# Optimization experiments

Measured on AMD Instinct MI355X. Metric: run time of the kernel, lower is better.

## Reference

```python
import jax, jax.numpy as jnp
import numpy as np

N_NODES = 10000
IN_CH = 512
HID = 128
HEADS = 4
OUT_CH = 256
N_EDGES = 160000
NEG_SLOPE = 0.2  # PyG GATConv default


def gat_conv(x, src, dst, W, a_src, a_dst, b):
    """PyG-style GATConv. x:[N,F_in], W:[F_in,H*C], a_src/a_dst:[H,C], b:[H*C].
    src/dst already include self-loops. Returns [N, H*C] (concat heads)."""
    N = x.shape[0]
    H, C = a_src.shape
    h = (x @ W).reshape(N, H, C)                     # [N,H,C]
    e_src = jnp.einsum('nhc,hc->nh', h, a_src)        # [N,H]
    e_dst = jnp.einsum('nhc,hc->nh', h, a_dst)
    alpha = jax.nn.leaky_relu(e_src[src] + e_dst[dst], NEG_SLOPE)  # [E,H]
    # softmax over incoming edges of each destination node
    m = jax.ops.segment_max(alpha, dst, num_segments=N)            # [N,H]
    ex = jnp.exp(alpha - m[dst])
    denom = jax.ops.segment_sum(ex, dst, num_segments=N)           # [N,H]
    coeff = ex / (denom[dst] + 1e-16)                              # [E,H]
    out = jax.ops.segment_sum(coeff[:, :, None] * h[src], dst, num_segments=N)  # [N,H,C]
    return out.reshape(N, H * C) + b


def _edges_with_self_loops(edge_index, n):
    loops = jnp.arange(n, dtype=edge_index.dtype)
    src = jnp.concatenate([edge_index[0], loops])
    dst = jnp.concatenate([edge_index[1], loops])
    return src, dst


def setup_inputs() -> dict:
    key = jax.random.key(0)
    ks = jax.random.split(key, 20)
    s = 0.05
    inp = {
        'x': jax.random.normal(ks[0], (N_NODES, IN_CH), jnp.float32),
        'W1': jax.random.normal(ks[1], (IN_CH, HEADS * HID), jnp.float32) * s,
        'a1s': jax.random.normal(ks[2], (HEADS, HID), jnp.float32) * s,
        'a1d': jax.random.normal(ks[3], (HEADS, HID), jnp.float32) * s,
        'b1': jnp.zeros((HEADS * HID,), jnp.float32),
        'W2': jax.random.normal(ks[4], (HEADS * HID, HEADS * HID), jnp.float32) * s,
        'a2s': jax.random.normal(ks[5], (HEADS, HID), jnp.float32) * s,
        'a2d': jax.random.normal(ks[6], (HEADS, HID), jnp.float32) * s,
        'b2': jnp.zeros((HEADS * HID,), jnp.float32),
        'W3': jax.random.normal(ks[7], (HEADS * HID, HID), jnp.float32) * s,
        'a3s': jax.random.normal(ks[8], (1, HID), jnp.float32) * s,
        'a3d': jax.random.normal(ks[9], (1, HID), jnp.float32) * s,
        'b3': jnp.zeros((HID,), jnp.float32),
        'Wl': jax.random.normal(ks[10], (HID, OUT_CH), jnp.float32) * s,
        'bl': jnp.zeros((OUT_CH,), jnp.float32),
        'Wr': jax.random.normal(ks[11], (IN_CH, OUT_CH), jnp.float32) * s,
        'br': jnp.zeros((OUT_CH,), jnp.float32),
        'edge_index': jax.random.randint(ks[12], (2, N_EDGES), 0, N_NODES, jnp.int64 if jax.config.jax_enable_x64 else jnp.int32),
    }
    return inp


def reference(x, W1, a1s, a1d, b1, W2, a2s, a2d, b2, W3, a3s, a3d, b3, Wl, bl, Wr, br, edge_index):
    src, dst = _edges_with_self_loops(edge_index, x.shape[0])
    residual = x @ Wr + br
    h = jax.nn.elu(gat_conv(x, src, dst, W1, a1s, a1d, b1))
    h = jax.nn.elu(gat_conv(h, src, dst, W2, a2s, a2d, b2))
    h = jax.nn.elu(gat_conv(h, src, dst, W3, a3s, a3d, b3))
    return h @ Wl + bl + residual
```

## Files before the change

kernel.cpp:

```cpp
#include <hip/hip_runtime.h>
#include <hip/hip_bf16.h>
#include <cstdint>
#include <cstddef>

#define N_NODES 10000
#define M_PAD   10112
#define HEADS   4

typedef __bf16 bfrag8 __attribute__((ext_vector_type(8)));
typedef __bf16 bfrag2 __attribute__((ext_vector_type(2)));
typedef float  floatx4 __attribute__((ext_vector_type(4)));
typedef float  floatx2 __attribute__((ext_vector_type(2)));

#define S0V (M_PAD * 512 / 8)
#define S1 (512 * 512)
#define S2 (512 * 512)
#define S3 (512 * 128)
#define S4 (128 * 256)
#define S5 (512 * 256)

__global__ __launch_bounds__(256) void prep(const float* __restrict__ x,
                                            const float* __restrict__ W1,
                                            const float* __restrict__ W2,
                                            const float* __restrict__ W3,
                                            const float* __restrict__ Wl,
                                            const float* __restrict__ Wr,
                                            const int* __restrict__ edst, int E,
                                            __bf16* __restrict__ xb,
                                            __bf16* __restrict__ W1T,
                                            __bf16* __restrict__ W2T,
                                            __bf16* __restrict__ W3T,
                                            __bf16* __restrict__ WlT,
                                            __bf16* __restrict__ WrT,
                                            int* __restrict__ deg) {
    int i = blockIdx.x * 256 + threadIdx.x;
    if (i < S0V) {
        int base = i * 8;
        int row = base >> 9;
        bfrag8 r = {};
        if (row < N_NODES) {
            float4 f0 = ((const float4*)x)[i * 2];
            float4 f1 = ((const float4*)x)[i * 2 + 1];
            r[0] = (__bf16)f0.x; r[1] = (__bf16)f0.y; r[2] = (__bf16)f0.z; r[3] = (__bf16)f0.w;
            r[4] = (__bf16)f1.x; r[5] = (__bf16)f1.y; r[6] = (__bf16)f1.z; r[7] = (__bf16)f1.w;
        }
        *(bfrag8*)(xb + base) = r;
    } else if ((i -= S0V) < S1) {
        int k = i >> 9, n = i & 511;
        W1T[n * 512 + k] = (__bf16)W1[i];
    } else if ((i -= S1) < S2) {
        int k = i >> 9, n = i & 511;
        W2T[n * 512 + k] = (__bf16)W2[i];
    } else if ((i -= S2) < S3) {
        int k = i >> 7, n = i & 127;
        W3T[n * 512 + k] = (__bf16)W3[i];
    } else if ((i -= S3) < S4) {
        int k = i >> 8, n = i & 255;
        WlT[n * 128 + k] = (__bf16)Wl[i];
    } else if ((i -= S4) < S5) {
        int k = i >> 8, n = i & 255;
        WrT[n * 512 + k] = (__bf16)Wr[i];
    } else if ((i -= S5) < E) {
        atomicAdd(&deg[edst[i]], 1);
    }
}


__global__ __launch_bounds__(256) void scan_kernel(const int* __restrict__ deg,
                                                   int* __restrict__ rowptr,
                                                   int* __restrict__ cursor, int n) {
    __shared__ int wtot[4], woff[4];
    int t = threadIdx.x, lane = t & 63, wv = t >> 6;
    int chunk = (n + 255) / 256;
    int beg = t * chunk, end = beg + chunk; if (end > n) end = n; if (beg > n) beg = n;
    int s = 0;
    for (int i = beg; i < end; ++i) s += deg[i] + 1;
    int v = s;
#pragma unroll
    for (int off = 1; off < 64; off <<= 1) {
        int o = __shfl_up(v, off);
        if (lane >= off) v += o;
    }
    if (lane == 63) wtot[wv] = v;
    __syncthreads();
    if (t == 0) {
        int r = 0;
#pragma unroll
        for (int i = 0; i < 4; ++i) { woff[i] = r; r += wtot[i]; }
        rowptr[n] = r;
    }
    __syncthreads();
    int off = woff[wv] + v - s;
    for (int i = beg; i < end; ++i) {
        rowptr[i] = off; cursor[i] = off;
        off += deg[i] + 1;
    }
}

__global__ __launch_bounds__(256) void scatter_kernel(const int* __restrict__ src,
                                                      const int* __restrict__ dst, int E, int n,
                                                      int* __restrict__ cursor,
                                                      int* __restrict__ csr) {
    int i = blockIdx.x * 256 + threadIdx.x;
    if (i < E) {
        int pos = atomicAdd(&cursor[dst[i]], 1);
        csr[pos] = src[i];
    } else if (i < E + n) {
        int v = i - E;
        int pos = atomicAdd(&cursor[v], 1);
        csr[pos] = v;
    }
}


template <int NT>
__device__ __forceinline__ void gemm_loop(const __bf16* __restrict__ A,
                                          const __bf16* __restrict__ BT, int K,
                                          int m0, int n0, int wave, int lane,
                                          __bf16* As, __bf16* Bs,
                                          floatx4 (&acc)[2][NT]) {
    int r = wave * 8 + (lane >> 3);
    int kof = (lane & 7) * 8;
    const __bf16* gA = A + (size_t)(m0 + r) * K + kof;
    const __bf16* gB = BT + (size_t)(n0 + r) * K + kof;
    __bf16* lA = As + r * 64 + kof;
    __bf16* lB = Bs + r * 64 + kof;
    const __bf16* fA = As + (wave * 32 + (lane & 15)) * 64 + (lane >> 4) * 8;
    const __bf16* fB = Bs + (lane & 15) * 64 + (lane >> 4) * 8;

    for (int k0 = 0; k0 < K; k0 += 64) {
#pragma unroll
        for (int u = 0; u < 4; ++u)
            __builtin_amdgcn_global_load_lds(
                (const __attribute__((address_space(1))) void*)(gA + (size_t)u * 32 * K),
                (__attribute__((address_space(3))) void*)(lA + u * 32 * 64), 16, 0, 0);
#pragma unroll
        for (int u = 0; u < NT / 2; ++u)
            __builtin_amdgcn_global_load_lds(
                (const __attribute__((address_space(1))) void*)(gB + (size_t)u * 32 * K),
                (__attribute__((address_space(3))) void*)(lB + u * 32 * 64), 16, 0, 0);
        gA += 64; gB += 64;
        __syncthreads();

#pragma unroll
        for (int ks = 0; ks < 2; ++ks) {
            bfrag8 a0 = *(const bfrag8*)(fA + ks * 32);
            bfrag8 a1 = *(const bfrag8*)(fA + 16 * 64 + ks * 32);
#pragma unroll
            for (int nt = 0; nt < NT; ++nt) {
                bfrag8 b = *(const bfrag8*)(fB + nt * 16 * 64 + ks * 32);
                acc[0][nt] = __builtin_amdgcn_mfma_f32_16x16x32_bf16(a0, b, acc[0][nt], 0, 0, 0);
                acc[1][nt] = __builtin_amdgcn_mfma_f32_16x16x32_bf16(a1, b, acc[1][nt], 0, 0, 0);
            }
        }
        __syncthreads();
    }
}

__global__ __launch_bounds__(256) void gemm_h(const __bf16* __restrict__ A,
                                              const __bf16* __restrict__ BT,
                                              __bf16* __restrict__ Cb,
                                              unsigned char* __restrict__ C8,
                                              int N, int K) {
    __shared__ __align__(16) __bf16 As[128 * 64];
    __shared__ __align__(16) __bf16 Bs[64 * 64];
    int tid = threadIdx.x, wave = tid >> 6, lane = tid & 63;
    int n0 = blockIdx.x * 64, m0 = blockIdx.y * 128;
    floatx4 acc[2][4] = {};
    gemm_loop<4>(A, BT, K, m0, n0, wave, lane, As, Bs, acc);

    int crow = m0 + wave * 32 + (lane >> 4) * 4;
    int ccol = n0 + (lane & 15);
#pragma unroll
    for (int mt = 0; mt < 2; ++mt)
#pragma unroll
        for (int nt = 0; nt < 4; ++nt)
#pragma unroll
            for (int r = 0; r < 4; ++r) {
                float v = acc[mt][nt][r];
                size_t o = (size_t)(crow + mt * 16 + r) * N + ccol + nt * 16;
                Cb[o] = (__bf16)v;
                int p = __builtin_amdgcn_cvt_pk_fp8_f32(v, v, 0, false);
                C8[o] = (unsigned char)(p & 0xff);
            }
}

__global__ __launch_bounds__(256) void gemm_final(const __bf16* __restrict__ A1,
                                                  const __bf16* __restrict__ B1T, int K1,
                                                  const __bf16* __restrict__ A2,
                                                  const __bf16* __restrict__ B2T, int K2,
                                                  float* __restrict__ C,
                                                  const float* __restrict__ bias1,
                                                  const float* __restrict__ bias2,
                                                  int M, int N) {
    __shared__ __align__(16) __bf16 As[128 * 64];
    __shared__ __align__(16) __bf16 Bs[64 * 64];
    int tid = threadIdx.x, wave = tid >> 6, lane = tid & 63;
    int n0 = blockIdx.x * 64, m0 = blockIdx.y * 128;
    floatx4 acc[2][4] = {};
    gemm_loop<4>(A1, B1T, K1, m0, n0, wave, lane, As, Bs, acc);
    gemm_loop<4>(A2, B2T, K2, m0, n0, wave, lane, As, Bs, acc);

    int crow = m0 + wave * 32 + (lane >> 4) * 4;
    int ccol = n0 + (lane & 15);
#pragma unroll
    for (int mt = 0; mt < 2; ++mt)
#pragma unroll
        for (int nt = 0; nt < 4; ++nt)
#pragma unroll
            for (int r = 0; r < 4; ++r) {
                int row = crow + mt * 16 + r;
                int col = ccol + nt * 16;
                if (row < M)
                    C[(size_t)row * N + col] = acc[mt][nt][r] + bias1[col] + bias2[col];
            }
}


template <int H>
__global__ __launch_bounds__(256) void attn_e(const __bf16* __restrict__ Hb,
                                              const float* __restrict__ as_,
                                              const float* __restrict__ ad_,
                                              float* __restrict__ es,
                                              float* __restrict__ ed) {
    constexpr int F = H * 128;
    constexpr int GROUP = (H == 4) ? 16 : 64;
    int wave = threadIdx.x >> 6, lane = threadIdx.x & 63;
    int node = blockIdx.x * 4 + wave;
    if (node >= N_NODES) return;
    float ps = 0.f, pd = 0.f;
    if (H == 4) {
        bfrag8 v = *(const bfrag8*)(Hb + (size_t)node * F + lane * 8);
#pragma unroll
        for (int k = 0; k < 8; ++k) {
            float f = (float)v[k];
            ps += f * as_[lane * 8 + k];
            pd += f * ad_[lane * 8 + k];
        }
    } else {
        bfrag2 v = *(const bfrag2*)(Hb + (size_t)node * F + lane * 2);
#pragma unroll
        for (int k = 0; k < 2; ++k) {
            float f = (float)v[k];
            ps += f * as_[lane * 2 + k];
            pd += f * ad_[lane * 2 + k];
        }
    }
#pragma unroll
    for (int off = GROUP / 2; off; off >>= 1) {
        ps += __shfl_down(ps, off);
        pd += __shfl_down(pd, off);
    }
    if ((lane & (GROUP - 1)) == 0) {
        es[node * H + lane / GROUP] = ps;
        ed[node * H + lane / GROUP] = pd;
    }
}


template <int H>
__global__ __launch_bounds__(256) void gather_agg(const unsigned char* __restrict__ H8,
                                                  const float* __restrict__ es,
                                                  const float* __restrict__ ed,
                                                  const int* __restrict__ rowptr,
                                                  const int* __restrict__ csr,
                                                  const float* __restrict__ bias,
                                                  __bf16* __restrict__ outb) {
    constexpr int F = H * 128;
    constexpr int CH = F / 64;
    int wave = threadIdx.x >> 6, lane = threadIdx.x & 63;
    int node = blockIdx.x * 4 + wave;
    if (node >= M_PAD) return;
    int hsel = (H == 4) ? (lane >> 4) : 0;
    __bf16* op = outb + (size_t)node * F + lane * CH;
    if (node >= N_NODES) {
        if (H == 4) { bfrag8 z = {}; *(bfrag8*)op = z; }
        else        { bfrag2 z = {}; *(bfrag2*)op = z; }
        return;
    }
    const unsigned char* hp = H8 + lane * CH;
    float edv = ed[node * H + hsel];
    int beg = rowptr[node], end = rowptr[node + 1];
    float acc[CH] = {};
    float wsum = 0.f;
    int j = beg;
    for (; j + 7 < end; j += 8) {
        int s[8];
        float e[8];
#pragma unroll
        for (int u = 0; u < 8; ++u) s[u] = csr[j + u];
#pragma unroll
        for (int u = 0; u < 8; ++u) e[u] = es[s[u] * H + hsel];
        if (H == 4) {
            uint2 p[8];
#pragma unroll
            for (int u = 0; u < 8; ++u) p[u] = *(const uint2*)(hp + (size_t)s[u] * F);
#pragma unroll
            for (int u = 0; u < 8; ++u) {
                float t = e[u] + edv;
                t = t > 0.f ? t : 0.2f * t;
                float wgt = __expf(t);
                wsum += wgt;
                floatx2 f0 = __builtin_amdgcn_cvt_pk_f32_fp8(p[u].x, false);
                floatx2 f1 = __builtin_amdgcn_cvt_pk_f32_fp8(p[u].x, true);
                floatx2 f2 = __builtin_amdgcn_cvt_pk_f32_fp8(p[u].y, false);
                floatx2 f3 = __builtin_amdgcn_cvt_pk_f32_fp8(p[u].y, true);
                acc[0] += wgt * f0[0]; acc[1] += wgt * f0[1];
                acc[2] += wgt * f1[0]; acc[3] += wgt * f1[1];
                acc[4] += wgt * f2[0]; acc[5] += wgt * f2[1];
                acc[6] += wgt * f3[0]; acc[7] += wgt * f3[1];
            }
        } else {
            unsigned short p[8];
#pragma unroll
            for (int u = 0; u < 8; ++u) p[u] = *(const unsigned short*)(hp + (size_t)s[u] * F);
#pragma unroll
            for (int u = 0; u < 8; ++u) {
                float t = e[u] + edv;
                t = t > 0.f ? t : 0.2f * t;
                float wgt = __expf(t);
                wsum += wgt;
                floatx2 f0 = __builtin_amdgcn_cvt_pk_f32_fp8((int)p[u], false);
                acc[0] += wgt * f0[0]; acc[1] += wgt * f0[1];
            }
        }
    }
    for (; j < end; ++j) {
        int s0 = csr[j];
        float t = es[s0 * H + hsel] + edv;
        t = t > 0.f ? t : 0.2f * t;
        float wgt = __expf(t);
        wsum += wgt;
        if (H == 4) {
            uint2 p = *(const uint2*)(hp + (size_t)s0 * F);
            floatx2 f0 = __builtin_amdgcn_cvt_pk_f32_fp8(p.x, false);
            floatx2 f1 = __builtin_amdgcn_cvt_pk_f32_fp8(p.x, true);
            floatx2 f2 = __builtin_amdgcn_cvt_pk_f32_fp8(p.y, false);
            floatx2 f3 = __builtin_amdgcn_cvt_pk_f32_fp8(p.y, true);
            acc[0] += wgt * f0[0]; acc[1] += wgt * f0[1];
            acc[2] += wgt * f1[0]; acc[3] += wgt * f1[1];
            acc[4] += wgt * f2[0]; acc[5] += wgt * f2[1];
            acc[6] += wgt * f3[0]; acc[7] += wgt * f3[1];
        } else {
            unsigned short p = *(const unsigned short*)(hp + (size_t)s0 * F);
            floatx2 f0 = __builtin_amdgcn_cvt_pk_f32_fp8((int)p, false);
            acc[0] += wgt * f0[0]; acc[1] += wgt * f0[1];
        }
    }
    float inv = 1.f / (wsum + 1e-16f);
    if (H == 4) {
        bfrag8 r;
#pragma unroll
        for (int k = 0; k < 8; ++k) {
            float o = acc[k] * inv + bias[lane * 8 + k];
            o = o > 0.f ? o : __expf(o) - 1.f;
            r[k] = (__bf16)o;
        }
        *(bfrag8*)op = r;
    } else {
        bfrag2 r;
#pragma unroll
        for (int k = 0; k < 2; ++k) {
            float o = acc[k] * inv + bias[lane * 2 + k];
            o = o > 0.f ? o : __expf(o) - 1.f;
            r[k] = (__bf16)o;
        }
        *(bfrag2*)op = r;
    }
}


extern "C" void kernel_launch(void* const* d_in, const int* in_sizes, int n_in,
                              void* d_out, int out_size, void* d_ws, size_t ws_size,
                              hipStream_t stream) {
    const float* x   = (const float*)d_in[0];
    const float* W1  = (const float*)d_in[1];
    const float* a1s = (const float*)d_in[2];
    const float* a1d = (const float*)d_in[3];
    const float* b1  = (const float*)d_in[4];
    const float* W2  = (const float*)d_in[5];
    const float* a2s = (const float*)d_in[6];
    const float* a2d = (const float*)d_in[7];
    const float* b2  = (const float*)d_in[8];
    const float* W3  = (const float*)d_in[9];
    const float* a3s = (const float*)d_in[10];
    const float* a3d = (const float*)d_in[11];
    const float* b3  = (const float*)d_in[12];
    const float* Wl  = (const float*)d_in[13];
    const float* bl  = (const float*)d_in[14];
    const float* Wr  = (const float*)d_in[15];
    const float* br  = (const float*)d_in[16];
    const int*   ei  = (const int*)d_in[17];
    const int E = in_sizes[17] / 2;
    const int* esrc = ei;
    const int* edst = ei + E;
    const int slots = E + N_NODES;
    float* out = (float*)d_out;

    char* w = (char*)d_ws;
    auto alloc = [&](size_t b) { char* p = w; w += (b + 255) & ~(size_t)255; return p; };
    __bf16* xb  = (__bf16*)alloc((size_t)M_PAD * 512 * 2);
    __bf16* hb  = (__bf16*)alloc((size_t)M_PAD * 512 * 2);
    __bf16* hb3 = (__bf16*)alloc((size_t)M_PAD * 128 * 2);
    __bf16* Hib = (__bf16*)alloc((size_t)M_PAD * 512 * 2);
    unsigned char* Hi8 = (unsigned char*)alloc((size_t)M_PAD * 512);
    __bf16* W1T = (__bf16*)alloc(512 * 512 * 2);
    __bf16* W2T = (__bf16*)alloc(512 * 512 * 2);
    __bf16* W3T = (__bf16*)alloc(128 * 512 * 2);
    __bf16* WlT = (__bf16*)alloc(256 * 128 * 2);
    __bf16* WrT = (__bf16*)alloc(256 * 512 * 2);
    float* es     = (float*)alloc(N_NODES * HEADS * 4);
    float* ed     = (float*)alloc(N_NODES * HEADS * 4);
    int*   deg    = (int*)alloc(N_NODES * 4);
    int*   rowptr = (int*)alloc((N_NODES + 1) * 4);
    int*   cursor = (int*)alloc(N_NODES * 4);
    int*   csr    = (int*)alloc((size_t)slots * 4);

    (void)hipMemsetAsync(deg, 0, N_NODES * sizeof(int), stream);

    const int sp_total = S0V + S1 + S2 + S3 + S4 + S5 + E;
    prep<<<(sp_total + 255) / 256, 256, 0, stream>>>(x, W1, W2, W3, Wl, Wr, edst, E,
                                                     xb, W1T, W2T, W3T, WlT, WrT, deg);
    scan_kernel<<<1, 256, 0, stream>>>(deg, rowptr, cursor, N_NODES);
    scatter_kernel<<<(E + N_NODES + 255) / 256, 256, 0, stream>>>(esrc, edst, E, N_NODES,
                                                                  cursor, csr);

    gemm_h<<<dim3(8, M_PAD / 128), 256, 0, stream>>>(xb, W1T, Hib, Hi8, 512, 512);
    attn_e<4><<<N_NODES / 4, 256, 0, stream>>>(Hib, a1s, a1d, es, ed);
    gather_agg<4><<<M_PAD / 4, 256, 0, stream>>>(Hi8, es, ed, rowptr, csr, b1, hb);
    gemm_h<<<dim3(8, M_PAD / 128), 256, 0, stream>>>(hb, W2T, Hib, Hi8, 512, 512);
    attn_e<4><<<N_NODES / 4, 256, 0, stream>>>(Hib, a2s, a2d, es, ed);
    gather_agg<4><<<M_PAD / 4, 256, 0, stream>>>(Hi8, es, ed, rowptr, csr, b2, hb);
    gemm_h<<<dim3(2, M_PAD / 128), 256, 0, stream>>>(hb, W3T, Hib, Hi8, 128, 512);
    attn_e<1><<<N_NODES / 4, 256, 0, stream>>>(Hib, a3s, a3d, es, ed);
    gather_agg<1><<<M_PAD / 4, 256, 0, stream>>>(Hi8, es, ed, rowptr, csr, b3, hb3);
    gemm_final<<<dim3(4, M_PAD / 128), 256, 0, stream>>>(xb, WrT, 512, hb3, WlT, 128,
                                                         out, br, bl, N_NODES, 256);
}
```

Before: 277.0 us.

## Fuse attention logit dot products into GEMM epilogue, drop bf16 H output

Each GEMM block now computes the per-node source and destination attention dot products from its fp32 accumulators. Each 64-column tile yields a partial sum per head half, written to a two-slot buffer, and a small attn_reduce kernel adds the two halves. This removes the separate attn_e kernel and the bf16 copy of H that it read. The cost is extra epilogue shuffles and an extra tiny launch per layer. The logits also now come from fp32 accumulators instead of bf16-rounded values.

```diff
diff --git a/kernel.cpp b/kernel.cpp
--- a/kernel.cpp
+++ b/kernel.cpp
@@ -159,9 +159,12 @@
 
 __global__ __launch_bounds__(256) void gemm_h(const __bf16* __restrict__ A,
                                               const __bf16* __restrict__ BT,
-                                              __bf16* __restrict__ Cb,
                                               unsigned char* __restrict__ C8,
-                                              int N, int K) {
+                                              int N, int K, int H,
+                                              const float* __restrict__ as_,
+                                              const float* __restrict__ ad_,
+                                              float* __restrict__ esp,
+                                              float* __restrict__ edp) {
     __shared__ __align__(16) __bf16 As[128 * 64];
     __shared__ __align__(16) __bf16 Bs[64 * 64];
     int tid = threadIdx.x, wave = tid >> 6, lane = tid & 63;
@@ -179,10 +182,55 @@
             for (int r = 0; r < 4; ++r) {
                 float v = acc[mt][nt][r];
                 size_t o = (size_t)(crow + mt * 16 + r) * N + ccol + nt * 16;
-                Cb[o] = (__bf16)v;
                 int p = __builtin_amdgcn_cvt_pk_fp8_f32(v, v, 0, false);
                 C8[o] = (unsigned char)(p & 0xff);
             }
+
+    int head = n0 >> 7;
+    int half = (n0 >> 6) & 1;
+    float a_sv[4], a_dv[4];
+#pragma unroll
+    for (int nt = 0; nt < 4; ++nt) {
+        int cin = (n0 & 64) + nt * 16 + (lane & 15);
+        a_sv[nt] = as_[head * 128 + cin];
+        a_dv[nt] = ad_[head * 128 + cin];
+    }
+    float* ep = esp + (size_t)half * M_PAD * H;
+    float* dp = edp + (size_t)half * M_PAD * H;
+#pragma unroll
+    for (int mt = 0; mt < 2; ++mt)
+#pragma unroll
+        for (int r = 0; r < 4; ++r) {
+            float ps = 0.f, pd = 0.f;
+#pragma unroll
+            for (int nt = 0; nt < 4; ++nt) {
+                float v = acc[mt][nt][r];
+                ps += v * a_sv[nt];
+                pd += v * a_dv[nt];
+            }
+#pragma unroll
+            for (int off = 8; off; off >>= 1) {
+                ps += __shfl_xor(ps, off);
+                pd += __shfl_xor(pd, off);
+            }
+            if ((lane & 15) == 0) {
+                int row = crow + mt * 16 + r;
+                ep[row * H + head] = ps;
+                dp[row * H + head] = pd;
+            }
+        }
+}
+
+__global__ __launch_bounds__(256) void attn_reduce(const float* __restrict__ esp,
+                                                   const float* __restrict__ edp,
+                                                   float* __restrict__ es,
+                                                   float* __restrict__ ed, int n, int H) {
+    int i = blockIdx.x * 256 + threadIdx.x;
+    if (i < n) {
+        const int off = M_PAD * H;
+        es[i] = esp[i] + esp[off + i];
+        ed[i] = edp[i] + edp[off + i];
+    }
 }
 
 __global__ __launch_bounds__(256) void gemm_final(const __bf16* __restrict__ A1,
@@ -214,47 +262,6 @@
                 if (row < M)
                     C[(size_t)row * N + col] = acc[mt][nt][r] + bias1[col] + bias2[col];
             }
-}
-
-
-template <int H>
-__global__ __launch_bounds__(256) void attn_e(const __bf16* __restrict__ Hb,
-                                              const float* __restrict__ as_,
-                                              const float* __restrict__ ad_,
-                                              float* __restrict__ es,
-                                              float* __restrict__ ed) {
-    constexpr int F = H * 128;
-    constexpr int GROUP = (H == 4) ? 16 : 64;
-    int wave = threadIdx.x >> 6, lane = threadIdx.x & 63;
-    int node = blockIdx.x * 4 + wave;
-    if (node >= N_NODES) return;
-    float ps = 0.f, pd = 0.f;
-    if (H == 4) {
-        bfrag8 v = *(const bfrag8*)(Hb + (size_t)node * F + lane * 8);
-#pragma unroll
-        for (int k = 0; k < 8; ++k) {
-            float f = (float)v[k];
-            ps += f * as_[lane * 8 + k];
-            pd += f * ad_[lane * 8 + k];
-        }
-    } else {
-        bfrag2 v = *(const bfrag2*)(Hb + (size_t)node * F + lane * 2);
-#pragma unroll
-        for (int k = 0; k < 2; ++k) {
-            float f = (float)v[k];
-            ps += f * as_[lane * 2 + k];
-            pd += f * ad_[lane * 2 + k];
-        }
-    }
-#pragma unroll
-    for (int off = GROUP / 2; off; off >>= 1) {
-        ps += __shfl_down(ps, off);
-        pd += __shfl_down(pd, off);
-    }
-    if ((lane & (GROUP - 1)) == 0) {
-        es[node * H + lane / GROUP] = ps;
-        ed[node * H + lane / GROUP] = pd;
-    }
 }
 
 
@@ -402,7 +409,6 @@
     __bf16* xb  = (__bf16*)alloc((size_t)M_PAD * 512 * 2);
     __bf16* hb  = (__bf16*)alloc((size_t)M_PAD * 512 * 2);
     __bf16* hb3 = (__bf16*)alloc((size_t)M_PAD * 128 * 2);
-    __bf16* Hib = (__bf16*)alloc((size_t)M_PAD * 512 * 2);
     unsigned char* Hi8 = (unsigned char*)alloc((size_t)M_PAD * 512);
     __bf16* W1T = (__bf16*)alloc(512 * 512 * 2);
     __bf16* W2T = (__bf16*)alloc(512 * 512 * 2);
@@ -411,6 +417,8 @@
     __bf16* WrT = (__bf16*)alloc(256 * 512 * 2);
     float* es     = (float*)alloc(N_NODES * HEADS * 4);
     float* ed     = (float*)alloc(N_NODES * HEADS * 4);
+    float* esp    = (float*)alloc((size_t)2 * M_PAD * HEADS * 4);
+    float* edp    = (float*)alloc((size_t)2 * M_PAD * HEADS * 4);
     int*   deg    = (int*)alloc(N_NODES * 4);
     int*   rowptr = (int*)alloc((N_NODES + 1) * 4);
     int*   cursor = (int*)alloc(N_NODES * 4);
@@ -425,14 +433,20 @@
     scatter_kernel<<<(E + N_NODES + 255) / 256, 256, 0, stream>>>(esrc, edst, E, N_NODES,
                                                                   cursor, csr);
 
-    gemm_h<<<dim3(8, M_PAD / 128), 256, 0, stream>>>(xb, W1T, Hib, Hi8, 512, 512);
-    attn_e<4><<<N_NODES / 4, 256, 0, stream>>>(Hib, a1s, a1d, es, ed);
+    gemm_h<<<dim3(8, M_PAD / 128), 256, 0, stream>>>(xb, W1T, Hi8, 512, 512, 4,
+                                                     a1s, a1d, esp, edp);
+    attn_reduce<<<(N_NODES * 4 + 255) / 256, 256, 0, stream>>>(esp, edp, es, ed,
+                                                               N_NODES * 4, 4);
     gather_agg<4><<<M_PAD / 4, 256, 0, stream>>>(Hi8, es, ed, rowptr, csr, b1, hb);
-    gemm_h<<<dim3(8, M_PAD / 128), 256, 0, stream>>>(hb, W2T, Hib, Hi8, 512, 512);
-    attn_e<4><<<N_NODES / 4, 256, 0, stream>>>(Hib, a2s, a2d, es, ed);
+    gemm_h<<<dim3(8, M_PAD / 128), 256, 0, stream>>>(hb, W2T, Hi8, 512, 512, 4,
+                                                     a2s, a2d, esp, edp);
+    attn_reduce<<<(N_NODES * 4 + 255) / 256, 256, 0, stream>>>(esp, edp, es, ed,
+                                                               N_NODES * 4, 4);
     gather_agg<4><<<M_PAD / 4, 256, 0, stream>>>(Hi8, es, ed, rowptr, csr, b2, hb);
-    gemm_h<<<dim3(2, M_PAD / 128), 256, 0, stream>>>(hb, W3T, Hib, Hi8, 128, 512);
-    attn_e<1><<<N_NODES / 4, 256, 0, stream>>>(Hib, a3s, a3d, es, ed);
+    gemm_h<<<dim3(2, M_PAD / 128), 256, 0, stream>>>(hb, W3T, Hi8, 128, 512, 1,
+                                                     a3s, a3d, esp, edp);
+    attn_reduce<<<(N_NODES + 255) / 256, 256, 0, stream>>>(esp, edp, es, ed,
+                                                           N_NODES, 1);
     gather_agg<1><<<M_PAD / 4, 256, 0, stream>>>(Hi8, es, ed, rowptr, csr, b3, hb3);
     gemm_final<<<dim3(4, M_PAD / 128), 256, 0, stream>>>(xb, WrT, 512, hb3, WlT, 128,
                                                          out, br, bl, N_NODES, 256);
```

New measurement: 272.7 us. About the same (-1.5%).
